# Optimization experiments

Hardware: AMD Instinct MI355X
Metric: run time of the kernel (lower is better)

## Reference

```python
import jax, jax.numpy as jnp
import numpy as np
import math

B, S, D = 4, 2048, 1024
H = 16
DH = D // H  # 64
DFF = 4096
EPS = 1e-5


def layernorm(x, g, b):
    mu = jnp.mean(x, axis=-1, keepdims=True)
    var = jnp.var(x, axis=-1, keepdims=True)
    return (x - mu) * jax.lax.rsqrt(var + EPS) * g + b


def setup_inputs() -> dict:
    key = jax.random.key(0)
    ks = jax.random.split(key, 16)
    s = 0.02
    return {
        "src": jax.random.normal(ks[0], (B, S, D), jnp.float32),
        # per-head q/k/v projections stacked: [H, D, DH]
        "Wq": jax.random.normal(ks[1], (H, D, DH), jnp.float32) * s,
        "bq": jnp.zeros((H, DH), jnp.float32),
        "Wk": jax.random.normal(ks[2], (H, D, DH), jnp.float32) * s,
        "bk": jnp.zeros((H, DH), jnp.float32),
        "Wv": jax.random.normal(ks[3], (H, D, DH), jnp.float32) * s,
        "bv": jnp.zeros((H, DH), jnp.float32),
        "Wo": jax.random.normal(ks[4], (D, D), jnp.float32) * s,
        "bo": jnp.zeros((D,), jnp.float32),
        "ln1_g": jnp.ones((D,), jnp.float32),
        "ln1_b": jnp.zeros((D,), jnp.float32),
        "W1": jax.random.normal(ks[5], (D, DFF), jnp.float32) * s,
        "b1": jnp.zeros((DFF,), jnp.float32),
        "W2": jax.random.normal(ks[6], (DFF, D), jnp.float32) * s,
        "b2": jnp.zeros((D,), jnp.float32),
        "ln2_g": jnp.ones((D,), jnp.float32),
        "ln2_b": jnp.zeros((D,), jnp.float32),
    }


def reference(src, Wq, bq, Wk, bk, Wv, bv, Wo, bo, ln1_g, ln1_b,
              W1, b1, W2, b2, ln2_g, ln2_b):
    # Batched equivalent of the per-head Python loop (no causal mask: mask=False)
    q = jnp.einsum('bsd,hde->bhse', src, Wq) + bq[None, :, None, :]
    k = jnp.einsum('bsd,hde->bhse', src, Wk) + bk[None, :, None, :]
    v = jnp.einsum('bsd,hde->bhse', src, Wv) + bv[None, :, None, :]
    scores = jnp.einsum('bhse,bhte->bhst', q, k) / math.sqrt(DH)
    attn = jax.nn.softmax(scores, axis=-1)
    ctx = jnp.einsum('bhst,bhte->bhse', attn, v)  # [B,H,S,DH]
    # cat over heads on last dim == transpose then merge
    ctx = ctx.transpose(0, 2, 1, 3).reshape(B, S, D)
    attn_out = ctx @ Wo + bo
    x1 = layernorm(attn_out + src, ln1_g, ln1_b)
    ffn = jax.nn.relu(x1 @ W1 + b1) @ W2 + b2
    return layernorm(ffn + x1, ln2_g, ln2_b)
```

## Files before the change

kernel.cpp:

```cpp
#include <hip/hip_runtime.h>
#include <stdint.h>

#define DEV __device__ __forceinline__

typedef float f32x4 __attribute__((ext_vector_type(4)));
typedef float f32x16 __attribute__((ext_vector_type(16)));
typedef __bf16 bf16x8 __attribute__((ext_vector_type(8)));
typedef __bf16 bf16x4 __attribute__((ext_vector_type(4)));
typedef unsigned short u16x4 __attribute__((ext_vector_type(4)));
typedef unsigned short u16x8 __attribute__((ext_vector_type(8)));
typedef unsigned u32x4 __attribute__((ext_vector_type(4)));

DEV unsigned short f2bf(float f) {
  unsigned u = __builtin_bit_cast(unsigned, f);
  u += 0x7fffu + ((u >> 16) & 1u);
  return (unsigned short)(u >> 16);
}
DEV float bf2f(unsigned short h) {
  unsigned u = ((unsigned)h) << 16;
  return __builtin_bit_cast(float, u);
}
DEV unsigned pkbf(float lo, float hi) {
  unsigned r;
  asm("v_cvt_pk_bf16_f32 %0, %1, %2" : "=v"(r) : "v"(lo), "v"(hi));
  return r;
}
DEV void gload_lds16(const void* g, void* l) {
  __builtin_amdgcn_global_load_lds((const __attribute__((address_space(1))) void*)g,
                                   (__attribute__((address_space(3))) void*)l, 16, 0, 0);
}

__global__ void cvt_f32_bf16(const float* __restrict__ in, unsigned short* __restrict__ out, int n) {
  int i = (blockIdx.x * 256 + threadIdx.x) * 4;
  if (i >= n) return;
  f32x4 v = *(const f32x4*)(in + i);
  u16x4 o;
  o[0] = f2bf(v[0]); o[1] = f2bf(v[1]); o[2] = f2bf(v[2]); o[3] = f2bf(v[3]);
  *(u16x4*)(out + i) = o;
}

__global__ void transpose_cvt(const float* __restrict__ src, unsigned short* __restrict__ dst,
                              int R, int C) {
  __shared__ __align__(16) float t[64][65];
  const int tid = threadIdx.x;
  const int r0 = blockIdx.x * 64, c0 = blockIdx.y * 64;
  const int rr = tid >> 2, q = tid & 3;
  const float* s = src + (size_t)(r0 + rr) * C + c0 + q * 16;
#pragma unroll
  for (int j = 0; j < 4; ++j) {
    f32x4 v = *(const f32x4*)(s + j * 4);
    t[rr][q * 16 + j * 4 + 0] = v[0];
    t[rr][q * 16 + j * 4 + 1] = v[1];
    t[rr][q * 16 + j * 4 + 2] = v[2];
    t[rr][q * 16 + j * 4 + 3] = v[3];
  }
  __syncthreads();
  const int cc = tid >> 2, qq = tid & 3;
  unsigned short* o = dst + (size_t)(c0 + cc) * R + r0 + qq * 16;
  u16x8 a, b;
#pragma unroll
  for (int j = 0; j < 8; ++j) {
    a[j] = f2bf(t[qq * 16 + j][cc]);
    b[j] = f2bf(t[qq * 16 + 8 + j][cc]);
  }
  *(u16x8*)o = a;
  *(u16x8*)(o + 8) = b;
}

__global__ void pack_qkv_w(const float* __restrict__ Wq, const float* __restrict__ Wk,
                           const float* __restrict__ Wv, unsigned short* __restrict__ dst) {
  __shared__ __align__(16) float t[64][65];
  const int tid = threadIdx.x;
  const int z = blockIdx.z, part = z >> 4, h = z & 15;
  const float* src = (part == 0 ? Wq : (part == 1 ? Wk : Wv)) + (size_t)h * 65536;
  const int r0 = blockIdx.x * 64;
  const int rr = tid >> 2, q = tid & 3;
  const float* s = src + (size_t)(r0 + rr) * 64 + q * 16;
#pragma unroll
  for (int j = 0; j < 4; ++j) {
    f32x4 v = *(const f32x4*)(s + j * 4);
    t[rr][q * 16 + j * 4 + 0] = v[0];
    t[rr][q * 16 + j * 4 + 1] = v[1];
    t[rr][q * 16 + j * 4 + 2] = v[2];
    t[rr][q * 16 + j * 4 + 3] = v[3];
  }
  __syncthreads();
  const int cc = tid >> 2, qq = tid & 3;
  unsigned short* o = dst + ((size_t)(part * 1024 + h * 64 + cc)) * 1024 + r0 + qq * 16;
  u16x8 a, b;
#pragma unroll
  for (int j = 0; j < 8; ++j) {
    a[j] = f2bf(t[qq * 16 + j][cc]);
    b[j] = f2bf(t[qq * 16 + 8 + j][cc]);
  }
  *(u16x8*)o = a;
  *(u16x8*)(o + 8) = b;
}

__global__ void pack_bias(const float* __restrict__ bq, const float* __restrict__ bk,
                          const float* __restrict__ bv, float* __restrict__ o) {
  int i = blockIdx.x * 256 + threadIdx.x;
  o[i] = i < 1024 ? bq[i] : (i < 2048 ? bk[i - 1024] : bv[i - 2048]);
}

__global__ void vtrans(const unsigned short* __restrict__ v, unsigned short* __restrict__ vt) {
  __shared__ __align__(16) unsigned short t[64][72];
  const int tid = threadIdx.x;
  const int bh = blockIdx.y, s0 = blockIdx.x * 64;
  const int r = tid >> 2, q = (tid & 3) * 16;
  const unsigned short* g = v + ((size_t)bh * 2048 + s0 + r) * 64 + q;
  *(u16x8*)&t[r][q] = *(const u16x8*)g;
  *(u16x8*)&t[r][q + 8] = *(const u16x8*)(g + 8);
  __syncthreads();
  const int d = tid >> 2, qq = (tid & 3) * 16;
  unsigned short* o = vt + ((size_t)bh * 64 + d) * 2048 + s0 + qq;
  u16x8 a, b;
#pragma unroll
  for (int j = 0; j < 8; ++j) {
    a[j] = t[qq + j][d];
    b[j] = t[qq + 8 + j][d];
  }
  *(u16x8*)o = a;
  *(u16x8*)(o + 8) = b;
}

template <int MODE>
__global__ __launch_bounds__(256, 2) void gemm_bt(
    const unsigned short* __restrict__ A, const unsigned short* __restrict__ Bt,
    const float* __restrict__ bias, unsigned short* __restrict__ out,
    unsigned short* __restrict__ qb, unsigned short* __restrict__ kb,
    unsigned short* __restrict__ vb, int M, int N, int K) {
  __shared__ __align__(16) char As[16384];
  __shared__ __align__(16) char Bs[16384];
  const int tid = threadIdx.x;
  const int wave = tid >> 6, lane = tid & 63;
  const int lrow = lane & 15;
  const int kof = (lane >> 4) * 16;
  const int m0 = blockIdx.y * 128, n0 = blockIdx.x * 128;
  const int wm = (wave >> 1) * 64, wn = (wave & 1) * 64;
  const int chunkrow = lane >> 3;
  const int colb0 = (lane & 7) * 16;

  f32x4 acc[4][4] = {};

  for (int k0 = 0; k0 < K; k0 += 64) {
#pragma unroll
    for (int c = 0; c < 4; ++c) {
      const int chunk = wave * 4 + c;
      const int rowA = chunk * 8 + chunkrow;
      const int srcb = colb0 ^ ((rowA & 7) << 4);
      const char* ga = (const char*)A + ((size_t)(m0 + rowA) * K + k0) * 2 + srcb;
      const char* gb = (const char*)Bt + ((size_t)(n0 + rowA) * K + k0) * 2 + srcb;
      gload_lds16(ga, As + chunk * 1024);
      gload_lds16(gb, Bs + chunk * 1024);
    }
    __syncthreads();
#pragma unroll
    for (int kk = 0; kk < 2; ++kk) {
      bf16x8 af[4], bv4[4];
#pragma unroll
      for (int i = 0; i < 4; ++i) {
        const int ra = wm + i * 16 + lrow;
        af[i] = *(const bf16x8*)(As + ra * 128 + ((kk * 64 + kof) ^ ((ra & 7) << 4)));
        const int rb = wn + i * 16 + lrow;
        bv4[i] = *(const bf16x8*)(Bs + rb * 128 + ((kk * 64 + kof) ^ ((rb & 7) << 4)));
      }
#pragma unroll
      for (int mi = 0; mi < 4; ++mi)
#pragma unroll
        for (int ni = 0; ni < 4; ++ni)
          acc[mi][ni] = __builtin_amdgcn_mfma_f32_16x16x32_bf16(af[mi], bv4[ni], acc[mi][ni], 0, 0, 0);
    }
    __syncthreads();
  }

#pragma unroll
  for (int mi = 0; mi < 4; ++mi) {
    const int row = m0 + wm + mi * 16 + ((lane >> 4) << 2);
#pragma unroll
    for (int ni = 0; ni < 4; ++ni) {
      const int col = n0 + wn + ni * 16 + lrow;
      const float bvv = bias[col];
#pragma unroll
      for (int r = 0; r < 4; ++r) {
        float v = acc[mi][ni][r] + bvv;
        if (MODE == 1) v = fmaxf(v, 0.0f);
        const int rr = row + r;
        if constexpr (MODE == 2) {
          const int part = col >> 10, cc = col & 1023, h = cc >> 6, e = cc & 63;
          if (part == 0) v *= 0.18033688011112042f;
          unsigned short* dst = part == 0 ? qb : (part == 1 ? kb : vb);
          dst[(((size_t)((rr >> 11) * 16 + h)) * 2048 + (rr & 2047)) * 64 + e] = f2bf(v);
        } else {
          out[(size_t)rr * N + col] = f2bf(v);
        }
      }
    }
  }
}

__global__ __launch_bounds__(256, 4) void attn_kernel(
    const unsigned short* __restrict__ q_buf, const unsigned short* __restrict__ k_buf,
    const unsigned short* __restrict__ vt_buf, unsigned short* __restrict__ ctx) {
  __shared__ __align__(16) char Ks[2][8192];
  __shared__ __align__(16) char Vs[2][8192];
  const int tid = threadIdx.x, wave = tid >> 6, lane = tid & 63;
  const int wg = (blockIdx.x & 7) * 128 + (blockIdx.x >> 3);
  const int bh = wg >> 4;
  const int q0 = (wg & 15) * 128;
  const int l31 = lane & 31, hi = lane >> 5;

  bf16x8 qf[4];
#pragma unroll
  for (int kk = 0; kk < 4; ++kk)
    qf[kk] = *(const bf16x8*)(q_buf +
        ((size_t)bh * 2048 + q0 + wave * 32 + l31) * 64 + kk * 16 + hi * 8);

  f32x16 acc_o[2] = {};
  float l_reg = 0.f;

  const int stg_r = tid >> 2;
  const int stg_p = (tid & 3) * 16;

  auto stage = [&](int t, int buf) {
#pragma unroll
    for (int i = 0; i < 2; ++i) {
      const int c = i * 256 + wave * 64 + lane;
      const int row = c >> 3;
      const int col = ((c & 7) * 16) ^ ((row & 7) << 4);
      gload_lds16((const char*)k_buf + ((size_t)(bh * 2048 + t * 64 + row)) * 128 + col,
                  &Ks[buf][(i * 256 + wave * 64) * 16]);
      gload_lds16((const char*)vt_buf + ((size_t)(bh * 64 + row)) * 4096 + t * 128 + col,
                  &Vs[buf][(i * 256 + wave * 64) * 16]);
    }
  };

  stage(0, 0);
  for (int t = 0; t < 32; ++t) {
    const int cur = t & 1;
    __syncthreads();
    stage(t < 31 ? t + 1 : 31, cur ^ 1);

    f32x16 sacc[2] = {};
#pragma unroll
    for (int kk = 0; kk < 4; ++kk) {
      bf16x8 kf[2];
#pragma unroll
      for (int mt = 0; mt < 2; ++mt) {
        const int row = mt * 32 + l31;
        kf[mt] = *(const bf16x8*)&Ks[cur][row * 128 + ((kk * 32 + hi * 16) ^ ((row & 7) << 4))];
      }
      __builtin_amdgcn_s_setprio(1);
#pragma unroll
      for (int mt = 0; mt < 2; ++mt)
        sacc[mt] = __builtin_amdgcn_mfma_f32_32x32x16_bf16(kf[mt], qf[kk], sacc[mt], 0, 0, 0);
      __builtin_amdgcn_s_setprio(0);
    }

#pragma unroll
    for (int mt = 0; mt < 2; ++mt)
#pragma unroll
      for (int r = 0; r < 16; ++r)
        sacc[mt][r] = exp2f(sacc[mt][r]);
    {
      f32x4 s0 = {sacc[0][0], sacc[0][1], sacc[0][2], sacc[0][3]};
      f32x4 s1 = {sacc[0][4], sacc[0][5], sacc[0][6], sacc[0][7]};
      f32x4 s2 = {sacc[0][8], sacc[0][9], sacc[0][10], sacc[0][11]};
      f32x4 s3 = {sacc[0][12], sacc[0][13], sacc[0][14], sacc[0][15]};
#pragma unroll
      for (int r = 0; r < 4; ++r) {
        s0[r] += sacc[1][r];  s1[r] += sacc[1][4 + r];
        s2[r] += sacc[1][8 + r];  s3[r] += sacc[1][12 + r];
      }
      f32x4 s01 = s0 + s1, s23 = s2 + s3;
      f32x4 sa = s01 + s23;
      l_reg += (sa[0] + sa[1]) + (sa[2] + sa[3]);
    }

#pragma unroll
    for (int g = 0; g < 4; ++g) {
      const int m = g >> 1, c = g & 1;
      unsigned w0 = pkbf(sacc[m][8 * c + 0], sacc[m][8 * c + 1]);
      unsigned w1 = pkbf(sacc[m][8 * c + 2], sacc[m][8 * c + 3]);
      unsigned w2 = pkbf(sacc[m][8 * c + 4], sacc[m][8 * c + 5]);
      unsigned w3 = pkbf(sacc[m][8 * c + 6], sacc[m][8 * c + 7]);
      u32x4 bw = {w0, w1, w2, w3};
      bf16x8 pb = __builtin_bit_cast(bf16x8, bw);
      bf16x8 vf[2];
#pragma unroll
      for (int mtd = 0; mtd < 2; ++mtd) {
        const int row = mtd * 32 + l31;
        const int cb = g * 32 + hi * 8;
        const int sw = (row & 7) << 4;
        bf16x4 lo = *(const bf16x4*)&Vs[cur][row * 128 + (cb ^ sw)];
        bf16x4 hi4 = *(const bf16x4*)&Vs[cur][row * 128 + ((cb + 16) ^ sw)];
        vf[mtd] = __builtin_shufflevector(lo, hi4, 0, 1, 2, 3, 4, 5, 6, 7);
      }
      __builtin_amdgcn_s_setprio(1);
#pragma unroll
      for (int mtd = 0; mtd < 2; ++mtd)
        acc_o[mtd] = __builtin_amdgcn_mfma_f32_32x32x16_bf16(vf[mtd], pb, acc_o[mtd], 0, 0, 0);
      __builtin_amdgcn_s_setprio(0);
    }
  }

  const float den = l_reg + __shfl_xor(l_reg, 32);
  const float inv = 1.0f / den;
  const int b = bh >> 4, h = bh & 15;
  const size_t orow = ((size_t)(b * 2048 + q0 + wave * 32 + l31)) * 1024 + h * 64;
#pragma unroll
  for (int mtd = 0; mtd < 2; ++mtd)
#pragma unroll
    for (int gq = 0; gq < 4; ++gq) {
      u16x4 o;
#pragma unroll
      for (int e = 0; e < 4; ++e) o[e] = f2bf(acc_o[mtd][gq * 4 + e] * inv);
      *(u16x4*)(ctx + orow + mtd * 32 + gq * 8 + hi * 4) = o;
    }
}

template <bool RES_BF, bool OUT_F32>
__global__ __launch_bounds__(256) void ln_kernel(
    const unsigned short* __restrict__ xin, const void* __restrict__ res,
    const float* __restrict__ g, const float* __restrict__ b, void* __restrict__ out) {
  const int row = blockIdx.x, tid = threadIdx.x;
  const size_t base = (size_t)row * 1024 + tid * 4;
  float x[4];
  u16x4 xv = *(const u16x4*)(xin + base);
  if constexpr (RES_BF) {
    u16x4 rv = *(const u16x4*)((const unsigned short*)res + base);
#pragma unroll
    for (int j = 0; j < 4; ++j) x[j] = bf2f(xv[j]) + bf2f(rv[j]);
  } else {
    f32x4 rv = *(const f32x4*)((const float*)res + base);
#pragma unroll
    for (int j = 0; j < 4; ++j) x[j] = bf2f(xv[j]) + rv[j];
  }
  float s1 = 0.f, s2 = 0.f;
#pragma unroll
  for (int j = 0; j < 4; ++j) { s1 += x[j]; s2 += x[j] * x[j]; }
#pragma unroll
  for (int off = 32; off > 0; off >>= 1) {
    s1 += __shfl_down(s1, off);
    s2 += __shfl_down(s2, off);
  }
  __shared__ float red[8];
  const int wv = tid >> 6, ln = tid & 63;
  if (ln == 0) { red[wv] = s1; red[4 + wv] = s2; }
  __syncthreads();
  s1 = red[0] + red[1] + red[2] + red[3];
  s2 = red[4] + red[5] + red[6] + red[7];
  const float mu = s1 * (1.0f / 1024.0f);
  const float rs = rsqrtf(s2 * (1.0f / 1024.0f) - mu * mu + 1e-5f);
#pragma unroll
  for (int j = 0; j < 4; ++j) {
    const float y = (x[j] - mu) * rs * g[tid * 4 + j] + b[tid * 4 + j];
    if constexpr (OUT_F32) ((float*)out)[base + j] = y;
    else ((unsigned short*)out)[base + j] = f2bf(y);
  }
}

static const size_t OFF_SBF  = 0;
static const size_t OFF_Q    = 16777216;
static const size_t OFF_K    = 33554432;
static const size_t OFF_V    = 50331648;
static const size_t OFF_VT   = 67108864;
static const size_t OFF_WQKV = 83886080;
static const size_t OFF_BQKV = 90177536;
static const size_t OFF_WO   = 90189824;
static const size_t OFF_W1   = 92286976;
static const size_t OFF_W2   = 100675584;
static const size_t OFF_CTX  = 109064192;
static const size_t OFF_AO   = 125841408;
static const size_t OFF_X1   = 142618624;
static const size_t OFF_FFN  = 159395840;

extern "C" void kernel_launch(void* const* d_in, const int* in_sizes, int n_in,
                              void* d_out, int out_size, void* d_ws, size_t ws_size,
                              hipStream_t stream) {
  const float* src = (const float*)d_in[0];
  const float* Wq  = (const float*)d_in[1];
  const float* bq  = (const float*)d_in[2];
  const float* Wk  = (const float*)d_in[3];
  const float* bk  = (const float*)d_in[4];
  const float* Wv  = (const float*)d_in[5];
  const float* bv  = (const float*)d_in[6];
  const float* Wo  = (const float*)d_in[7];
  const float* bo  = (const float*)d_in[8];
  const float* g1  = (const float*)d_in[9];
  const float* be1 = (const float*)d_in[10];
  const float* W1  = (const float*)d_in[11];
  const float* b1  = (const float*)d_in[12];
  const float* W2  = (const float*)d_in[13];
  const float* b2  = (const float*)d_in[14];
  const float* g2  = (const float*)d_in[15];
  const float* be2 = (const float*)d_in[16];

  char* ws = (char*)d_ws;
  unsigned short* sbf  = (unsigned short*)(ws + OFF_SBF);
  unsigned short* h1   = (unsigned short*)(ws + OFF_SBF);
  unsigned short* qb   = (unsigned short*)(ws + OFF_Q);
  unsigned short* kb   = (unsigned short*)(ws + OFF_K);
  unsigned short* vb   = (unsigned short*)(ws + OFF_V);
  unsigned short* vtb  = (unsigned short*)(ws + OFF_VT);
  unsigned short* wqkv = (unsigned short*)(ws + OFF_WQKV);
  float*          bqkv = (float*)(ws + OFF_BQKV);
  unsigned short* wot  = (unsigned short*)(ws + OFF_WO);
  unsigned short* w1t  = (unsigned short*)(ws + OFF_W1);
  unsigned short* w2t  = (unsigned short*)(ws + OFF_W2);
  unsigned short* ctx  = (unsigned short*)(ws + OFF_CTX);
  unsigned short* ao   = (unsigned short*)(ws + OFF_AO);
  unsigned short* x1   = (unsigned short*)(ws + OFF_X1);
  unsigned short* ffn  = (unsigned short*)(ws + OFF_FFN);
  float* outp = (float*)d_out;

  cvt_f32_bf16<<<dim3(8192), dim3(256), 0, stream>>>(src, sbf, 8388608);
  pack_qkv_w<<<dim3(16, 1, 48), dim3(256), 0, stream>>>(Wq, Wk, Wv, wqkv);
  pack_bias<<<dim3(12), dim3(256), 0, stream>>>(bq, bk, bv, bqkv);
  transpose_cvt<<<dim3(16, 16), dim3(256), 0, stream>>>(Wo, wot, 1024, 1024);
  transpose_cvt<<<dim3(16, 64), dim3(256), 0, stream>>>(W1, w1t, 1024, 4096);
  transpose_cvt<<<dim3(64, 16), dim3(256), 0, stream>>>(W2, w2t, 4096, 1024);

  gemm_bt<2><<<dim3(24, 64), dim3(256), 0, stream>>>(sbf, wqkv, bqkv, nullptr, qb, kb, vb,
                                                     8192, 3072, 1024);
  vtrans<<<dim3(32, 64), dim3(256), 0, stream>>>(vb, vtb);
  attn_kernel<<<dim3(1024), dim3(256), 0, stream>>>(qb, kb, vtb, ctx);
  gemm_bt<0><<<dim3(8, 64), dim3(256), 0, stream>>>(ctx, wot, bo, ao, nullptr, nullptr, nullptr,
                                                    8192, 1024, 1024);
  ln_kernel<false, false><<<dim3(8192), dim3(256), 0, stream>>>(ao, src, g1, be1, x1);
  gemm_bt<1><<<dim3(32, 64), dim3(256), 0, stream>>>(x1, w1t, b1, h1, nullptr, nullptr, nullptr,
                                                     8192, 4096, 1024);
  gemm_bt<0><<<dim3(8, 64), dim3(256), 0, stream>>>(h1, w2t, b2, ffn, nullptr, nullptr, nullptr,
                                                    8192, 1024, 4096);
  ln_kernel<true, true><<<dim3(8192), dim3(256), 0, stream>>>(ffn, x1, g2, be2, outp);

  (void)in_sizes; (void)n_in; (void)out_size; (void)ws_size;
}
```

Baseline: 389.2 us.

## Compute softmax denominator via MFMA, raw v_exp, permuted V layout, higher GEMM occupancy

The attention kernel now accumulates the softmax row sums with an extra MFMA against a vector of ones, replacing the VALU reduction. It also calls v_exp_f32 directly instead of exp2f and reads V fragments with a single 8-wide LDS load, with vtrans permuting its output so the new load order stays consistent. GEMM launch bounds go from 2 to 3 waves per SIMD, and the first LayerNorm reads the bf16 copy of src instead of fp32. Together these cut VALU work and memory traffic, at the cost of extra MFMA issue, register pressure from the tighter bounds, and a residual rounded to bf16.

```diff
diff --git a/kernel.cpp b/kernel.cpp
--- a/kernel.cpp
+++ b/kernel.cpp
@@ -23,6 +23,11 @@
 DEV unsigned pkbf(float lo, float hi) {
   unsigned r;
   asm("v_cvt_pk_bf16_f32 %0, %1, %2" : "=v"(r) : "v"(lo), "v"(hi));
+  return r;
+}
+DEV float fexp2(float x) {
+  float r;
+  asm("v_exp_f32 %0, %1" : "=v"(r) : "v"(x));
   return r;
 }
 DEV void gload_lds16(const void* g, void* l) {
@@ -117,15 +122,16 @@
   u16x8 a, b;
 #pragma unroll
   for (int j = 0; j < 8; ++j) {
-    a[j] = t[qq + j][d];
-    b[j] = t[qq + 8 + j][d];
+    const int sa = (j & 3) | ((j & 4) << 1);
+    a[j] = t[qq + sa][d];
+    b[j] = t[qq + sa + 4][d];
   }
   *(u16x8*)o = a;
   *(u16x8*)(o + 8) = b;
 }
 
 template <int MODE>
-__global__ __launch_bounds__(256, 2) void gemm_bt(
+__global__ __launch_bounds__(256, 3) void gemm_bt(
     const unsigned short* __restrict__ A, const unsigned short* __restrict__ Bt,
     const float* __restrict__ bias, unsigned short* __restrict__ out,
     unsigned short* __restrict__ qb, unsigned short* __restrict__ kb,
@@ -217,10 +223,10 @@
         ((size_t)bh * 2048 + q0 + wave * 32 + l31) * 64 + kk * 16 + hi * 8);
 
   f32x16 acc_o[2] = {};
-  float l_reg = 0.f;
-
-  const int stg_r = tid >> 2;
-  const int stg_p = (tid & 3) * 16;
+  f32x16 accd = {};
+  bf16x8 ones;
+#pragma unroll
+  for (int j = 0; j < 8; ++j) ones[j] = (__bf16)1.0f;
 
   auto stage = [&](int t, int buf) {
 #pragma unroll
@@ -261,21 +267,7 @@
     for (int mt = 0; mt < 2; ++mt)
 #pragma unroll
       for (int r = 0; r < 16; ++r)
-        sacc[mt][r] = exp2f(sacc[mt][r]);
-    {
-      f32x4 s0 = {sacc[0][0], sacc[0][1], sacc[0][2], sacc[0][3]};
-      f32x4 s1 = {sacc[0][4], sacc[0][5], sacc[0][6], sacc[0][7]};
-      f32x4 s2 = {sacc[0][8], sacc[0][9], sacc[0][10], sacc[0][11]};
-      f32x4 s3 = {sacc[0][12], sacc[0][13], sacc[0][14], sacc[0][15]};
-#pragma unroll
-      for (int r = 0; r < 4; ++r) {
-        s0[r] += sacc[1][r];  s1[r] += sacc[1][4 + r];
-        s2[r] += sacc[1][8 + r];  s3[r] += sacc[1][12 + r];
-      }
-      f32x4 s01 = s0 + s1, s23 = s2 + s3;
-      f32x4 sa = s01 + s23;
-      l_reg += (sa[0] + sa[1]) + (sa[2] + sa[3]);
-    }
+        sacc[mt][r] = fexp2(sacc[mt][r]);
 
 #pragma unroll
     for (int g = 0; g < 4; ++g) {
@@ -290,13 +282,11 @@
 #pragma unroll
       for (int mtd = 0; mtd < 2; ++mtd) {
         const int row = mtd * 32 + l31;
-        const int cb = g * 32 + hi * 8;
         const int sw = (row & 7) << 4;
-        bf16x4 lo = *(const bf16x4*)&Vs[cur][row * 128 + (cb ^ sw)];
-        bf16x4 hi4 = *(const bf16x4*)&Vs[cur][row * 128 + ((cb + 16) ^ sw)];
-        vf[mtd] = __builtin_shufflevector(lo, hi4, 0, 1, 2, 3, 4, 5, 6, 7);
+        vf[mtd] = *(const bf16x8*)&Vs[cur][row * 128 + ((g * 32 + hi * 16) ^ sw)];
       }
       __builtin_amdgcn_s_setprio(1);
+      accd = __builtin_amdgcn_mfma_f32_32x32x16_bf16(ones, pb, accd, 0, 0, 0);
 #pragma unroll
       for (int mtd = 0; mtd < 2; ++mtd)
         acc_o[mtd] = __builtin_amdgcn_mfma_f32_32x32x16_bf16(vf[mtd], pb, acc_o[mtd], 0, 0, 0);
@@ -304,8 +294,7 @@
     }
   }
 
-  const float den = l_reg + __shfl_xor(l_reg, 32);
-  const float inv = 1.0f / den;
+  const float inv = 1.0f / accd[0];
   const int b = bh >> 4, h = bh & 15;
   const size_t orow = ((size_t)(b * 2048 + q0 + wave * 32 + l31)) * 1024 + h * 64;
 #pragma unroll
@@ -427,7 +416,7 @@
   attn_kernel<<<dim3(1024), dim3(256), 0, stream>>>(qb, kb, vtb, ctx);
   gemm_bt<0><<<dim3(8, 64), dim3(256), 0, stream>>>(ctx, wot, bo, ao, nullptr, nullptr, nullptr,
                                                     8192, 1024, 1024);
-  ln_kernel<false, false><<<dim3(8192), dim3(256), 0, stream>>>(ao, src, g1, be1, x1);
+  ln_kernel<true, false><<<dim3(8192), dim3(256), 0, stream>>>(ao, sbf, g1, be1, x1);
   gemm_bt<1><<<dim3(32, 64), dim3(256), 0, stream>>>(x1, w1t, b1, h1, nullptr, nullptr, nullptr,
                                                      8192, 4096, 1024);
   gemm_bt<0><<<dim3(8, 64), dim3(256), 0, stream>>>(h1, w2t, b2, ffn, nullptr, nullptr, nullptr,
```

New measurement: 370.3 us. 1.05x faster.
